# Kernel tuning notes

Hardware: AMD Instinct MI355X
Metric: run time of the kernel (lower is better)

Reference implementation:

```python
import jax, jax.numpy as jnp
import numpy as np

B, C, L, K = 64, 2, 131072, 4


def setup_inputs() -> dict:
    key = jax.random.key(0)
    k1, k2, k3, k4 = jax.random.split(key, 4)
    x = jax.random.normal(k1, (B, C, L), dtype=jnp.float32)
    Bs = 0.5 * jax.random.normal(k2, (B, C, K, 3), dtype=jnp.float32)
    # Build stable denominators: complex-conjugate poles r*exp(+-j*theta), r < 0.95
    # a(z) = 1 - 2 r cos(theta) z^-1 + r^2 z^-2  -> guaranteed-stable IIR cascade.
    r = jax.random.uniform(k3, (B, C, K), minval=0.1, maxval=0.95)
    theta = jax.random.uniform(k4, (B, C, K), minval=0.05, maxval=np.pi - 0.05)
    a1 = -2.0 * r * jnp.cos(theta)
    a2 = r * r
    As = jnp.stack([jnp.ones_like(a1), a1, a2], axis=-1).astype(jnp.float32)
    return {"input_signal": x, "Bs": Bs, "As": As}


def _biquad_cascade(x, b, a):
    # x: [N, L]; b, a: [N, K, 3] with a already normalized (a0 == 1).
    # Serial cascade of K biquads, each in direct form II transposed:
    #   y[n]  = b0*u[n] + s1
    #   s1'   = b1*u[n] - a1*y[n] + s2
    #   s2'   = b2*u[n] - a2*y[n]
    # Exactly the linear recurrence the ssm/lfilter backends compute.
    nK = b.shape[1]
    b0, b1, b2 = b[..., 0], b[..., 1], b[..., 2]  # each [N, K]
    a1, a2 = a[..., 1], a[..., 2]

    def step(carry, xt):
        s1, s2 = carry  # each [N, K]
        u = xt  # [N]
        s1n, s2n = [], []
        for k in range(nK):  # small fixed cascade depth, unrolled
            y = b0[:, k] * u + s1[:, k]
            s1n.append(b1[:, k] * u - a1[:, k] * y + s2[:, k])
            s2n.append(b2[:, k] * u - a2[:, k] * y)
            u = y
        return (jnp.stack(s1n, axis=1), jnp.stack(s2n, axis=1)), u

    N = x.shape[0]
    init = (jnp.zeros((N, nK), x.dtype), jnp.zeros((N, nK), x.dtype))
    _, ys = jax.lax.scan(step, init, x.T)  # scan over time: ys [L, N]
    return ys.T


def reference(input_signal, Bs, As):
    b, c, audio_len = input_signal.shape
    assert Bs.shape[-1] == As.shape[-1] == 3
    # channel broadcasting as in _process_ssm
    if c == 1 and Bs.shape[1] > 1:
        input_signal = jnp.broadcast_to(input_signal, (b, Bs.shape[1], audio_len))
        c = Bs.shape[1]
    elif Bs.shape[1] == 1 and c > 1:
        Bs = jnp.broadcast_to(Bs, (b, c) + Bs.shape[2:])
        As = jnp.broadcast_to(As, (b, c) + As.shape[2:])
    a0 = As[..., :1]
    Bn = (Bs / a0).reshape(b * c, -1, 3)
    An = (As / a0).reshape(b * c, -1, 3)
    x = input_signal.reshape(b * c, audio_len)
    y = _biquad_cascade(x, Bn, An)
    return y.reshape(b, c, audio_len)
```

## Files before the change

### kernel.cpp

```cpp
#include <hip/hip_runtime.h>
#include <hip/hip_cooperative_groups.h>
#include <math.h>

namespace cg = cooperative_groups;


#define SS   64
#define WMAX 384
#define WMIN 64
#define TT   32
#define TPB  256
#define LSTR 33
#define KB   4
#define NL   8
#define HALO 6
#define DSTR 9

typedef float vf4 __attribute__((ext_vector_type(4)));

__global__ void iir_prep2_kernel(const float* __restrict__ Bs,
                                 const float* __restrict__ As, int rows,
                                 int* __restrict__ nwrow,
                                 float* __restrict__ nmat,
                                 float* __restrict__ wmat)
{
    __shared__ float mat[4][5][64];
    const int grp  = threadIdx.x >> 6;
    const int lane = threadIdx.x & 63;
    const int row  = blockIdx.x * 4 + grp;
    const bool act = (row < rows);

    float b0[KB], b1[KB], b2[KB], na1[KB], na2[KB];
    if (act) {
        const float* Bp = Bs + (size_t)row * KB * 3;
        const float* Ap = As + (size_t)row * KB * 3;
#pragma unroll
        for (int k = 0; k < KB; ++k) {
            float inv = 1.0f / Ap[3 * k];
            b0[k]  =  Bp[3 * k]     * inv;
            b1[k]  =  Bp[3 * k + 1] * inv;
            b2[k]  =  Bp[3 * k + 2] * inv;
            na1[k] = -Ap[3 * k + 1] * inv;
            na2[k] = -Ap[3 * k + 2] * inv;
        }
    }

    float* cur = &mat[grp][0][0];
    float* nxt = &mat[grp][1][0];
    float* n1  = &mat[grp][2][0];
    float* ac  = &mat[grp][3][0];
    float* cw  = &mat[grp][4][0];

    if (act && lane < 8) {
        float s[8];
#pragma unroll
        for (int i = 0; i < 8; ++i) s[i] = (i == lane) ? 1.0f : 0.0f;
        float u = 0.0f;
#pragma unroll
        for (int k = 0; k < KB; ++k) {
            float y  = fmaf(b0[k], u, s[2 * k]);
            float t1 = fmaf(na1[k], y, fmaf(b1[k], u, s[2 * k + 1]));
            float t2 = fmaf(na2[k], y, b2[k] * u);
            s[2 * k] = t1; s[2 * k + 1] = t2; u = y;
        }
#pragma unroll
        for (int i = 0; i < 8; ++i) { cur[i * 8 + lane] = s[i]; ac[i * 8 + lane] = s[i]; }
        cw[lane] = u;
    }
    __syncthreads();

    const int i8 = lane >> 3, j8 = lane & 7;

    for (int t = 0; t < 6; ++t) {
        float acc = 0.0f;
        if (act) {
#pragma unroll
            for (int m = 0; m < 8; ++m)
                acc = fmaf(cur[i8 * 8 + m], cur[m * 8 + j8], acc);
            nxt[lane] = acc;
        }
        __syncthreads();
        float* t0 = cur; cur = nxt; nxt = t0;
    }

    if (act) {
        float v = cur[lane];
        n1[lane] = v;
        nmat[(size_t)row * 320 + lane] = v;
    }
    __syncthreads();

    for (int m = 2; m <= 5; ++m) {
        float acc = 0.0f;
        if (act) {
#pragma unroll
            for (int q = 0; q < 8; ++q)
                acc = fmaf(cur[i8 * 8 + q], n1[q * 8 + j8], acc);
            nxt[lane] = acc;
            nmat[(size_t)row * 320 + (m - 1) * 64 + lane] = acc;
        }
        __syncthreads();
        float* t0 = cur; cur = nxt; nxt = t0;
    }
    __syncthreads();

    if (act && lane < 8) {
        float Ac[8];
#pragma unroll
        for (int i = 0; i < 8; ++i) Ac[i] = ac[i * 8 + lane];
        float w = cw[lane];
        float* wm = wmat + (size_t)row * 512;
        for (int t = 0; t < SS; ++t) {
            wm[t * 8 + lane] = w;
            float acc = 0.0f;
#pragma unroll
            for (int i = 0; i < 8; ++i)
                acc = fmaf(__shfl(w, i, 8), Ac[i], acc);
            w = acc;
        }
    }

    if (act && lane == 0) {
        const float* Ap = As + (size_t)row * KB * 3;
        float r2max = 0.0f;
#pragma unroll
        for (int k = 0; k < KB; ++k) {
            float a0 = Ap[3 * k];
            float a2 = Ap[3 * k + 2] / a0;
            r2max = fmaxf(r2max, a2);
        }
        float rmax = fminf(fmaxf(sqrtf(fmaxf(r2max, 0.f)), 0.20f), 0.955f);
        float Wf = 25.6f / (-logf(rmax));
        int W = ((int)ceilf(Wf) + TT - 1) & ~(TT - 1);
        W = min(max(W, WMIN), WMAX);
        nwrow[row] = (W + SS - 1) / SS;
    }
}

__global__ __launch_bounds__(TPB, 4) void iir_fused_kernel(
    const float* __restrict__ x, const float* __restrict__ Bs,
    const float* __restrict__ As, float* __restrict__ out, int L,
    const float* __restrict__ nmat, const float* __restrict__ wmat,
    const int* __restrict__ nwrow, float* __restrict__ halo)
{
    __shared__ float lds[TPB * LSTR];
    const int tid = threadIdx.x;
    const int cpr = L / SS;
    const int bpr = cpr / TPB;
    const int row = blockIdx.x / bpr;
    const int blk = blockIdx.x % bpr;
    const int chunk0 = blk * TPB;

    float b0[KB], b1[KB], b2[KB], na1[KB], na2[KB];
    const float* Bp = Bs + (size_t)row * KB * 3;
    const float* Ap = As + (size_t)row * KB * 3;
#pragma unroll
    for (int k = 0; k < KB; ++k) {
        float inv = 1.0f / Ap[3 * k];
        b0[k]  =  Bp[3 * k]     * inv;
        b1[k]  =  Bp[3 * k + 1] * inv;
        b2[k]  =  Bp[3 * k + 2] * inv;
        na1[k] = -Ap[3 * k + 1] * inv;
        na2[k] = -Ap[3 * k + 2] * inv;
    }

    const float* xrow = x   + (size_t)row * L;
    float*       orow = out + (size_t)row * L;
    float*       myrow = lds + tid * LSTR;

    const int tq = tid >> 3;
    const int p4 = (tid & 7) << 2;
    int off[NL], ldsoff[NL];
#pragma unroll
    for (int l = 0; l < NL; ++l) {
        int j = l * 32 + tq;
        off[l]    = (chunk0 + j) * SS + p4;
        ldsoff[l] = j * LSTR + p4;
    }

    float y0[SS];
    float s1[KB] = {0.f, 0.f, 0.f, 0.f};
    float s2[KB] = {0.f, 0.f, 0.f, 0.f};

    float4 rn[NL];
#pragma unroll
    for (int l = 0; l < NL; ++l)
        rn[l] = *reinterpret_cast<const float4*>(xrow + off[l]);

#pragma unroll
    for (int it = 0; it < SS / TT; ++it) {
        __syncthreads();
#pragma unroll
        for (int l = 0; l < NL; ++l) {
            float* d = lds + ldsoff[l];
            d[0] = rn[l].x; d[1] = rn[l].y; d[2] = rn[l].z; d[3] = rn[l].w;
        }
        if (it + 1 < SS / TT) {
#pragma unroll
            for (int l = 0; l < NL; ++l)
                rn[l] = *reinterpret_cast<const float4*>(xrow + off[l] + (it + 1) * TT);
        }
        __syncthreads();

#pragma unroll
        for (int q = 0; q < TT; ++q) {
            float u = myrow[q];
#pragma unroll
            for (int k = 0; k < KB; ++k) {
                float yv = fmaf(b0[k], u, s1[k]);
                s1[k] = fmaf(na1[k], yv, fmaf(b1[k], u, s2[k]));
                s2[k] = fmaf(na2[k], yv, b2[k] * u);
                u = yv;
            }
            y0[it * TT + q] = u;
        }
    }

    __syncthreads();
    float* dl = lds;
#pragma unroll
    for (int k = 0; k < KB; ++k) {
        dl[(tid + HALO) * DSTR + 2 * k]     = s1[k];
        dl[(tid + HALO) * DSTR + 2 * k + 1] = s2[k];
    }
    if (tid >= TPB - HALO) {
        size_t hb = ((size_t)blockIdx.x * HALO + (tid - (TPB - HALO))) * 8;
#pragma unroll
        for (int k = 0; k < KB; ++k) {
            __hip_atomic_store(&halo[hb + 2 * k],     s1[k], __ATOMIC_RELEASE, __HIP_MEMORY_SCOPE_AGENT);
            __hip_atomic_store(&halo[hb + 2 * k + 1], s2[k], __ATOMIC_RELEASE, __HIP_MEMORY_SCOPE_AGENT);
        }
    }

    cg::this_grid().sync();

    if (tid < HALO) {
        float v[8] = {0.f, 0.f, 0.f, 0.f, 0.f, 0.f, 0.f, 0.f};
        if (blk > 0) {
            size_t hb = ((size_t)(blockIdx.x - 1) * HALO + tid) * 8;
#pragma unroll
            for (int i = 0; i < 8; ++i)
                v[i] = __hip_atomic_load(&halo[hb + i], __ATOMIC_ACQUIRE, __HIP_MEMORY_SCOPE_AGENT);
        }
#pragma unroll
        for (int i = 0; i < 8; ++i) dl[tid * DSTR + i] = v[i];
    }
    __syncthreads();

    const int nW = nwrow[row];
    const float* Nrow = nmat + (size_t)row * 320;
    const float* Wrow = wmat + (size_t)row * 512;
    float pst[8];
#pragma unroll
    for (int i = 0; i < 8; ++i) pst[i] = dl[(tid + HALO - 1) * DSTR + i];
#pragma unroll 1
    for (int m = 2; m <= nW; ++m) {
        const float* M  = Nrow + (m - 2) * 64;
        const float* dd = dl + (tid + HALO - m) * DSTR;
        float din[8];
#pragma unroll
        for (int q = 0; q < 8; ++q) din[q] = dd[q];
#pragma unroll
        for (int i = 0; i < 8; ++i) {
            float a = pst[i];
#pragma unroll
            for (int q = 0; q < 8; ++q) a = fmaf(M[i * 8 + q], din[q], a);
            pst[i] = a;
        }
    }

#pragma unroll
    for (int t = 0; t < SS; ++t) {
        float a = y0[t];
#pragma unroll
        for (int i = 0; i < 8; ++i) a = fmaf(Wrow[t * 8 + i], pst[i], a);
        y0[t] = a;
    }

#pragma unroll
    for (int it = 0; it < SS / TT; ++it) {
        __syncthreads();
#pragma unroll
        for (int q = 0; q < TT; ++q) myrow[q] = y0[it * TT + q];
        __syncthreads();
#pragma unroll
        for (int l = 0; l < NL; ++l) {
            const float* sp = lds + ldsoff[l];
            vf4 v = { sp[0], sp[1], sp[2], sp[3] };
            __builtin_nontemporal_store(
                v, reinterpret_cast<vf4*>(orow + off[l] + it * TT));
        }
    }
}

__global__ __launch_bounds__(TPB, 4) void iir_state_kernel(
    const float* __restrict__ x, const float* __restrict__ Bs,
    const float* __restrict__ As, int L, float* __restrict__ dstate)
{
    __shared__ float lds[TPB * LSTR];
    const int tid = threadIdx.x;
    const int cpr = L / SS;
    const int bpr = cpr / TPB;
    const int row = blockIdx.x / bpr;
    const int chunk0 = (blockIdx.x % bpr) * TPB;

    float b0[KB], b1[KB], b2[KB], na1[KB], na2[KB];
    const float* Bp = Bs + (size_t)row * KB * 3;
    const float* Ap = As + (size_t)row * KB * 3;
#pragma unroll
    for (int k = 0; k < KB; ++k) {
        float inv = 1.0f / Ap[3 * k];
        b0[k]  =  Bp[3 * k]     * inv;
        b1[k]  =  Bp[3 * k + 1] * inv;
        b2[k]  =  Bp[3 * k + 2] * inv;
        na1[k] = -Ap[3 * k + 1] * inv;
        na2[k] = -Ap[3 * k + 2] * inv;
    }

    float s1[KB] = {0.f, 0.f, 0.f, 0.f};
    float s2[KB] = {0.f, 0.f, 0.f, 0.f};

    const float* xrow = x + (size_t)row * L;
    float* myrow = lds + tid * LSTR;

    const int tq = tid >> 3;
    const int p4 = (tid & 7) << 2;
    int off[NL], ldsoff[NL];
#pragma unroll
    for (int l = 0; l < NL; ++l) {
        int j = l * 32 + tq;
        off[l]    = (chunk0 + j) * SS + p4;
        ldsoff[l] = j * LSTR + p4;
    }

    float4 rn[NL];
#pragma unroll
    for (int l = 0; l < NL; ++l)
        rn[l] = *reinterpret_cast<const float4*>(xrow + off[l]);

#pragma unroll
    for (int it = 0; it < SS / TT; ++it) {
        __syncthreads();
#pragma unroll
        for (int l = 0; l < NL; ++l) {
            float* d = lds + ldsoff[l];
            d[0] = rn[l].x; d[1] = rn[l].y; d[2] = rn[l].z; d[3] = rn[l].w;
        }
        if (it + 1 < SS / TT) {
            const int base = (it + 1) * TT;
#pragma unroll
            for (int l = 0; l < NL; ++l)
                rn[l] = *reinterpret_cast<const float4*>(xrow + off[l] + base);
        }
        __syncthreads();

#pragma unroll
        for (int p = 0; p < TT; ++p) {
            float u = myrow[p];
#pragma unroll
            for (int k = 0; k < KB; ++k) {
                float yv = fmaf(b0[k], u, s1[k]);
                s1[k] = fmaf(na1[k], yv, fmaf(b1[k], u, s2[k]));
                s2[k] = fmaf(na2[k], yv, b2[k] * u);
                u = yv;
            }
        }
    }

    float* dp = dstate + ((size_t)row * cpr + chunk0 + tid) * 8;
    float4 d0 = make_float4(s1[0], s2[0], s1[1], s2[1]);
    float4 d1 = make_float4(s1[2], s2[2], s1[3], s2[3]);
    *reinterpret_cast<float4*>(dp)     = d0;
    *reinterpret_cast<float4*>(dp + 4) = d1;
}

__global__ __launch_bounds__(TPB, 4) void iir_out_kernel(
    const float* __restrict__ x, const float* __restrict__ Bs,
    const float* __restrict__ As, float* __restrict__ out, int L,
    const float* __restrict__ dstate, const float* __restrict__ nmat,
    const int* __restrict__ nwrow)
{
    __shared__ float lds[TPB * LSTR];
    const int tid = threadIdx.x;
    const int cpr = L / SS;
    const int bpr = cpr / TPB;
    const int row = blockIdx.x / bpr;
    const int chunk0 = (blockIdx.x % bpr) * TPB;
    const int nW = nwrow[row];

    float b0[KB], b1[KB], b2[KB], na1[KB], na2[KB];
    const float* Bp = Bs + (size_t)row * KB * 3;
    const float* Ap = As + (size_t)row * KB * 3;
#pragma unroll
    for (int k = 0; k < KB; ++k) {
        float inv = 1.0f / Ap[3 * k];
        b0[k]  =  Bp[3 * k]     * inv;
        b1[k]  =  Bp[3 * k + 1] * inv;
        b2[k]  =  Bp[3 * k + 2] * inv;
        na1[k] = -Ap[3 * k + 1] * inv;
        na2[k] = -Ap[3 * k + 2] * inv;
    }

    const float* xrow = x   + (size_t)row * L;
    float*       orow = out + (size_t)row * L;
    float*       myrow = lds + tid * LSTR;

    const int tq = tid >> 3;
    const int p4 = (tid & 7) << 2;
    int off[NL], ldsoff[NL];
#pragma unroll
    for (int l = 0; l < NL; ++l) {
        int j = l * 32 + tq;
        off[l]    = (chunk0 + j) * SS + p4;
        ldsoff[l] = j * LSTR + p4;
    }

    float4 rn[NL];
#pragma unroll
    for (int l = 0; l < NL; ++l)
        rn[l] = *reinterpret_cast<const float4*>(xrow + off[l]);

    float* dl = lds;
    float* nl = lds + (TPB + HALO) * DSTR;
    const float* dbase = dstate + ((size_t)row * cpr + chunk0 - HALO) * 8;
    for (int e = tid; e < (TPB + HALO) * 8; e += TPB) {
        int c  = e >> 3;
        int gi = chunk0 - HALO + c;
        float v = 0.0f;
        if (gi >= 0) v = dbase[e];
        dl[c * DSTR + (e & 7)] = v;
    }
    for (int e = tid; e < 320; e += TPB) nl[e] = nmat[(size_t)row * 320 + e];
    __syncthreads();

    float p[8];
#pragma unroll
    for (int i = 0; i < 8; ++i) p[i] = dl[(tid + HALO - 1) * DSTR + i];
#pragma unroll 1
    for (int m = 2; m <= nW; ++m) {
        const float* M  = nl + (m - 2) * 64;
        const float* dd = dl + (tid + HALO - m) * DSTR;
        float din[8];
#pragma unroll
        for (int q = 0; q < 8; ++q) din[q] = dd[q];
#pragma unroll
        for (int i = 0; i < 8; ++i) {
            float a = p[i];
#pragma unroll
            for (int q = 0; q < 8; ++q) a = fmaf(M[i * 8 + q], din[q], a);
            p[i] = a;
        }
    }
    float s1[KB], s2[KB];
#pragma unroll
    for (int k = 0; k < KB; ++k) { s1[k] = p[2 * k]; s2[k] = p[2 * k + 1]; }

#pragma unroll
    for (int it = 0; it < SS / TT; ++it) {
        __syncthreads();
#pragma unroll
        for (int l = 0; l < NL; ++l) {
            float* d = lds + ldsoff[l];
            d[0] = rn[l].x; d[1] = rn[l].y; d[2] = rn[l].z; d[3] = rn[l].w;
        }
        if (it + 1 < SS / TT) {
            const int base = (it + 1) * TT;
#pragma unroll
            for (int l = 0; l < NL; ++l)
                rn[l] = *reinterpret_cast<const float4*>(xrow + off[l] + base);
        }
        __syncthreads();

#pragma unroll
        for (int q = 0; q < TT; ++q) {
            float u = myrow[q];
#pragma unroll
            for (int k = 0; k < KB; ++k) {
                float yv = fmaf(b0[k], u, s1[k]);
                s1[k] = fmaf(na1[k], yv, fmaf(b1[k], u, s2[k]));
                s2[k] = fmaf(na2[k], yv, b2[k] * u);
                u = yv;
            }
            myrow[q] = u;
        }
        __syncthreads();

        const int base = it * TT;
#pragma unroll
        for (int l = 0; l < NL; ++l) {
            const float* sp = lds + ldsoff[l];
            vf4 v = { sp[0], sp[1], sp[2], sp[3] };
            __builtin_nontemporal_store(
                v, reinterpret_cast<vf4*>(orow + off[l] + base));
        }
    }
}

__global__ void iir_prep_kernel(const float* __restrict__ As, int rows,
                                int* __restrict__ wrow, int* __restrict__ perm)
{
    __shared__ int sw[256];
    const int r = threadIdx.x;
    int W = 0;
    if (r < rows) {
        float r2max = 0.f;
#pragma unroll
        for (int k = 0; k < KB; ++k) {
            float a0 = As[(size_t)r * KB * 3 + 3 * k];
            float a2 = As[(size_t)r * KB * 3 + 3 * k + 2] / a0;
            r2max = fmaxf(r2max, a2);
        }
        float rmax = fminf(fmaxf(sqrtf(fmaxf(r2max, 0.f)), 0.20f), 0.955f);
        float Wf = 25.6f / (-logf(rmax));
        W = ((int)ceilf(Wf) + TT - 1) & ~(TT - 1);
        W = min(max(W, WMIN), WMAX);
        wrow[r] = W;
    }
    sw[r] = W;
    __syncthreads();
    if (r < rows) {
        int rank = 0;
        for (int i = 0; i < rows; ++i)
            rank += (sw[i] > W) || (sw[i] == W && i < r);
        perm[rank] = r;
    }
}

__global__ __launch_bounds__(TPB, 4) void iir_chunks_kernel(
    const float* __restrict__ x, const float* __restrict__ Bs,
    const float* __restrict__ As, float* __restrict__ out, int L,
    const int* __restrict__ wrow, const int* __restrict__ perm)
{
    __shared__ float lds[TPB * LSTR];
    const int tid = threadIdx.x;
    const int bpr = (L / SS) / TPB;
    const int row = perm[blockIdx.x / bpr];
    const int chunk0 = (blockIdx.x % bpr) * TPB;
    const int W = wrow[row];

    float b0[KB], b1[KB], b2[KB], na1[KB], na2[KB];
    const float* Bp = Bs + (size_t)row * KB * 3;
    const float* Ap = As + (size_t)row * KB * 3;
#pragma unroll
    for (int k = 0; k < KB; ++k) {
        float inv = 1.0f / Ap[3 * k];
        b0[k]  =  Bp[3 * k]     * inv;
        b1[k]  =  Bp[3 * k + 1] * inv;
        b2[k]  =  Bp[3 * k + 2] * inv;
        na1[k] = -Ap[3 * k + 1] * inv;
        na2[k] = -Ap[3 * k + 2] * inv;
    }

    float s1[KB] = {0.f, 0.f, 0.f, 0.f};
    float s2[KB] = {0.f, 0.f, 0.f, 0.f};

    const float* xrow = x   + (size_t)row * L;
    float*       orow = out + (size_t)row * L;
    float*       myrow = lds + tid * LSTR;

    const int tq = tid >> 3;
    const int p4 = (tid & 7) << 2;
    int off[NL], ldsoff[NL];
#pragma unroll
    for (int l = 0; l < NL; ++l) {
        int j = l * 32 + tq;
        off[l]    = (chunk0 + j) * SS + p4 - W;
        ldsoff[l] = j * LSTR + p4;
    }

    const int NT = (SS + W) / TT;
    const int WT = W / TT;

    float4 rn[NL];
#pragma unroll
    for (int l = 0; l < NL; ++l) {
        int pos = off[l];
        rn[l] = make_float4(0.f, 0.f, 0.f, 0.f);
        if (pos >= 0) rn[l] = *reinterpret_cast<const float4*>(xrow + pos);
    }

#pragma unroll 1
    for (int it = 0; it < NT; ++it) {
        __syncthreads();
#pragma unroll
        for (int l = 0; l < NL; ++l) {
            float* d = lds + ldsoff[l];
            d[0] = rn[l].x; d[1] = rn[l].y; d[2] = rn[l].z; d[3] = rn[l].w;
        }
        if (it + 1 < NT) {
            const int base = (it + 1) * TT;
#pragma unroll
            for (int l = 0; l < NL; ++l) {
                int pos = off[l] + base;
                rn[l] = make_float4(0.f, 0.f, 0.f, 0.f);
                if (pos >= 0) rn[l] = *reinterpret_cast<const float4*>(xrow + pos);
            }
        }
        __syncthreads();

        if (it < WT) {
#pragma unroll
            for (int p = 0; p < TT; ++p) {
                float u = myrow[p];
#pragma unroll
                for (int k = 0; k < KB; ++k) {
                    float yv = fmaf(b0[k], u, s1[k]);
                    s1[k] = fmaf(na1[k], yv, fmaf(b1[k], u, s2[k]));
                    s2[k] = fmaf(na2[k], yv, b2[k] * u);
                    u = yv;
                }
            }
        } else {
#pragma unroll
            for (int p = 0; p < TT; ++p) {
                float u = myrow[p];
#pragma unroll
                for (int k = 0; k < KB; ++k) {
                    float yv = fmaf(b0[k], u, s1[k]);
                    s1[k] = fmaf(na1[k], yv, fmaf(b1[k], u, s2[k]));
                    s2[k] = fmaf(na2[k], yv, b2[k] * u);
                    u = yv;
                }
                myrow[p] = u;
            }
            __syncthreads();

            const int base = it * TT - W;
#pragma unroll
            for (int l = 0; l < NL; ++l) {
                const float* sp = lds + ldsoff[l];
                vf4 v = { sp[0], sp[1], sp[2], sp[3] };
                __builtin_nontemporal_store(
                    v, reinterpret_cast<vf4*>(orow + off[l] + W + base));
            }
        }
    }
}

extern "C" void kernel_launch(void* const* d_in, const int* in_sizes, int n_in,
                              void* d_out, int out_size, void* d_ws, size_t ws_size,
                              hipStream_t stream) {
    const float* x  = (const float*)d_in[0];
    const float* Bs = (const float*)d_in[1];
    const float* As = (const float*)d_in[2];
    float* out = (float*)d_out;

    const int rows = in_sizes[1] / (KB * 3);
    const int L    = in_sizes[0] / rows;
    const int cpr  = L / SS;
    const int bpr  = cpr / TPB;
    const int grid = rows * bpr;

    float* dstate = (float*)d_ws;
    float* nmatp  = dstate + (size_t)rows * cpr * 8;
    float* wmatp  = nmatp  + (size_t)rows * 320;
    float* halop  = wmatp  + (size_t)rows * 512;
    int*   nwrowp = (int*)(halop + (size_t)grid * HALO * 8);
    const size_t need = (size_t)((char*)(nwrowp + rows) - (char*)d_ws);

    const bool shape_ok = (L % SS) == 0 && bpr * TPB == cpr && ws_size >= need;

    static int coopCap = -2;
    if (coopCap == -2) {
        int mb = 0, dev = 0, cus = 0;
        if (hipOccupancyMaxActiveBlocksPerMultiprocessor(&mb, iir_fused_kernel,
                                                         TPB, 0) != hipSuccess) mb = 0;
        hipGetDevice(&dev);
        if (hipDeviceGetAttribute(&cus, hipDeviceAttributeMultiprocessorCount,
                                  dev) != hipSuccess) cus = 0;
        coopCap = mb * cus;
    }

    if (shape_ok) {
        hipLaunchKernelGGL(iir_prep2_kernel, dim3((rows + 3) / 4), dim3(256), 0,
                           stream, Bs, As, rows, nwrowp, nmatp, wmatp);
        bool done = false;
        if (coopCap >= grid) {
            int Lv = L;
            void* args[] = { (void*)&x, (void*)&Bs, (void*)&As, (void*)&out,
                             (void*)&Lv, (void*)&nmatp, (void*)&wmatp,
                             (void*)&nwrowp, (void*)&halop };
            if (hipLaunchCooperativeKernel(iir_fused_kernel, dim3(grid), dim3(TPB),
                                           args, 0, stream) == hipSuccess)
                done = true;
        }
        if (!done) {
            hipLaunchKernelGGL(iir_state_kernel, dim3(grid), dim3(TPB), 0,
                               stream, x, Bs, As, L, dstate);
            hipLaunchKernelGGL(iir_out_kernel, dim3(grid), dim3(TPB), 0,
                               stream, x, Bs, As, out, L, dstate, nmatp, nwrowp);
        }
    } else {
        int* wrow = (int*)d_ws;
        int* perm = wrow + rows;
        hipLaunchKernelGGL(iir_prep_kernel, dim3(1), dim3(256), 0, stream,
                           As, rows, wrow, perm);
        hipLaunchKernelGGL(iir_chunks_kernel, dim3(rows * bpr), dim3(TPB), 0,
                           stream, x, Bs, As, out, L, wrow, perm);
    }
}
```

Measured before the change: 140.8 us.

## Recompute chunk outputs after grid sync instead of storing y0 and correction matrix

Result: faster. 133.9 us (-4.9%).

```diff
diff --git a/kernel.cpp b/kernel.cpp
--- a/kernel.cpp
+++ b/kernel.cpp
@@ -21,10 +21,9 @@
 __global__ void iir_prep2_kernel(const float* __restrict__ Bs,
                                  const float* __restrict__ As, int rows,
                                  int* __restrict__ nwrow,
-                                 float* __restrict__ nmat,
-                                 float* __restrict__ wmat)
+                                 float* __restrict__ nmat)
 {
-    __shared__ float mat[4][5][64];
+    __shared__ float mat[4][3][64];
     const int grp  = threadIdx.x >> 6;
     const int lane = threadIdx.x & 63;
     const int row  = blockIdx.x * 4 + grp;
@@ -48,8 +47,6 @@
     float* cur = &mat[grp][0][0];
     float* nxt = &mat[grp][1][0];
     float* n1  = &mat[grp][2][0];
-    float* ac  = &mat[grp][3][0];
-    float* cw  = &mat[grp][4][0];
 
     if (act && lane < 8) {
         float s[8];
@@ -64,8 +61,7 @@
             s[2 * k] = t1; s[2 * k + 1] = t2; u = y;
         }
 #pragma unroll
-        for (int i = 0; i < 8; ++i) { cur[i * 8 + lane] = s[i]; ac[i * 8 + lane] = s[i]; }
-        cw[lane] = u;
+        for (int i = 0; i < 8; ++i) cur[i * 8 + lane] = s[i];
     }
     __syncthreads();
 
@@ -101,23 +97,6 @@
         }
         __syncthreads();
         float* t0 = cur; cur = nxt; nxt = t0;
-    }
-    __syncthreads();
-
-    if (act && lane < 8) {
-        float Ac[8];
-#pragma unroll
-        for (int i = 0; i < 8; ++i) Ac[i] = ac[i * 8 + lane];
-        float w = cw[lane];
-        float* wm = wmat + (size_t)row * 512;
-        for (int t = 0; t < SS; ++t) {
-            wm[t * 8 + lane] = w;
-            float acc = 0.0f;
-#pragma unroll
-            for (int i = 0; i < 8; ++i)
-                acc = fmaf(__shfl(w, i, 8), Ac[i], acc);
-            w = acc;
-        }
     }
 
     if (act && lane == 0) {
@@ -140,8 +119,8 @@
 __global__ __launch_bounds__(TPB, 4) void iir_fused_kernel(
     const float* __restrict__ x, const float* __restrict__ Bs,
     const float* __restrict__ As, float* __restrict__ out, int L,
-    const float* __restrict__ nmat, const float* __restrict__ wmat,
-    const int* __restrict__ nwrow, float* __restrict__ halo)
+    const float* __restrict__ nmat, const int* __restrict__ nwrow,
+    float* __restrict__ halo)
 {
     __shared__ float lds[TPB * LSTR];
     const int tid = threadIdx.x;
@@ -178,7 +157,6 @@
         ldsoff[l] = j * LSTR + p4;
     }
 
-    float y0[SS];
     float s1[KB] = {0.f, 0.f, 0.f, 0.f};
     float s2[KB] = {0.f, 0.f, 0.f, 0.f};
 
@@ -196,15 +174,16 @@
             d[0] = rn[l].x; d[1] = rn[l].y; d[2] = rn[l].z; d[3] = rn[l].w;
         }
         if (it + 1 < SS / TT) {
+            const int base = (it + 1) * TT;
 #pragma unroll
             for (int l = 0; l < NL; ++l)
-                rn[l] = *reinterpret_cast<const float4*>(xrow + off[l] + (it + 1) * TT);
-        }
-        __syncthreads();
-
-#pragma unroll
-        for (int q = 0; q < TT; ++q) {
-            float u = myrow[q];
+                rn[l] = *reinterpret_cast<const float4*>(xrow + off[l] + base);
+        }
+        __syncthreads();
+
+#pragma unroll
+        for (int p = 0; p < TT; ++p) {
+            float u = myrow[p];
 #pragma unroll
             for (int k = 0; k < KB; ++k) {
                 float yv = fmaf(b0[k], u, s1[k]);
@@ -212,7 +191,6 @@
                 s2[k] = fmaf(na2[k], yv, b2[k] * u);
                 u = yv;
             }
-            y0[it * TT + q] = u;
         }
     }
 
@@ -231,6 +209,10 @@
             __hip_atomic_store(&halo[hb + 2 * k + 1], s2[k], __ATOMIC_RELEASE, __HIP_MEMORY_SCOPE_AGENT);
         }
     }
+
+#pragma unroll
+    for (int l = 0; l < NL; ++l)
+        rn[l] = *reinterpret_cast<const float4*>(xrow + off[l]);
 
     cg::this_grid().sync();
 
@@ -249,7 +231,6 @@
 
     const int nW = nwrow[row];
     const float* Nrow = nmat + (size_t)row * 320;
-    const float* Wrow = wmat + (size_t)row * 512;
     float pst[8];
 #pragma unroll
     for (int i = 0; i < 8; ++i) pst[i] = dl[(tid + HALO - 1) * DSTR + i];
@@ -268,27 +249,46 @@
             pst[i] = a;
         }
     }
-
-#pragma unroll
-    for (int t = 0; t < SS; ++t) {
-        float a = y0[t];
-#pragma unroll
-        for (int i = 0; i < 8; ++i) a = fmaf(Wrow[t * 8 + i], pst[i], a);
-        y0[t] = a;
-    }
+#pragma unroll
+    for (int k = 0; k < KB; ++k) { s1[k] = pst[2 * k]; s2[k] = pst[2 * k + 1]; }
 
 #pragma unroll
     for (int it = 0; it < SS / TT; ++it) {
         __syncthreads();
 #pragma unroll
-        for (int q = 0; q < TT; ++q) myrow[q] = y0[it * TT + q];
-        __syncthreads();
+        for (int l = 0; l < NL; ++l) {
+            float* d = lds + ldsoff[l];
+            d[0] = rn[l].x; d[1] = rn[l].y; d[2] = rn[l].z; d[3] = rn[l].w;
+        }
+        if (it + 1 < SS / TT) {
+            const int base = (it + 1) * TT;
+#pragma unroll
+            for (int l = 0; l < NL; ++l)
+                rn[l] = *reinterpret_cast<const float4*>(xrow + off[l] + base);
+        }
+        __syncthreads();
+
+#pragma unroll
+        for (int q = 0; q < TT; ++q) {
+            float u = myrow[q];
+#pragma unroll
+            for (int k = 0; k < KB; ++k) {
+                float yv = fmaf(b0[k], u, s1[k]);
+                s1[k] = fmaf(na1[k], yv, fmaf(b1[k], u, s2[k]));
+                s2[k] = fmaf(na2[k], yv, b2[k] * u);
+                u = yv;
+            }
+            myrow[q] = u;
+        }
+        __syncthreads();
+
+        const int base = it * TT;
 #pragma unroll
         for (int l = 0; l < NL; ++l) {
             const float* sp = lds + ldsoff[l];
             vf4 v = { sp[0], sp[1], sp[2], sp[3] };
             __builtin_nontemporal_store(
-                v, reinterpret_cast<vf4*>(orow + off[l] + it * TT));
+                v, reinterpret_cast<vf4*>(orow + off[l] + base));
         }
     }
 }
@@ -653,8 +653,7 @@
 
     float* dstate = (float*)d_ws;
     float* nmatp  = dstate + (size_t)rows * cpr * 8;
-    float* wmatp  = nmatp  + (size_t)rows * 320;
-    float* halop  = wmatp  + (size_t)rows * 512;
+    float* halop  = nmatp  + (size_t)rows * 320;
     int*   nwrowp = (int*)(halop + (size_t)grid * HALO * 8);
     const size_t need = (size_t)((char*)(nwrowp + rows) - (char*)d_ws);
 
@@ -673,13 +672,13 @@
 
     if (shape_ok) {
         hipLaunchKernelGGL(iir_prep2_kernel, dim3((rows + 3) / 4), dim3(256), 0,
-                           stream, Bs, As, rows, nwrowp, nmatp, wmatp);
+                           stream, Bs, As, rows, nwrowp, nmatp);
         bool done = false;
         if (coopCap >= grid) {
             int Lv = L;
             void* args[] = { (void*)&x, (void*)&Bs, (void*)&As, (void*)&out,
-                             (void*)&Lv, (void*)&nmatp, (void*)&wmatp,
-                             (void*)&nwrowp, (void*)&halop };
+                             (void*)&Lv, (void*)&nmatp, (void*)&nwrowp,
+                             (void*)&halop };
             if (hipLaunchCooperativeKernel(iir_fused_kernel, dim3(grid), dim3(TPB),
                                            args, 0, stream) == hipSuccess)
                 done = true;
```
